# Performance work log

Measured on AMD Instinct MI355X. Metric: run time of the kernel, lower is better.

## Reference

```python
import jax, jax.numpy as jnp
import numpy as np

LAMBDA = 25.0
MU = 25.0
NU = 1.0
ALPHA = 0.25
EPS = 1e-4
NUM_MATCHES = (20, 4)


def _cdist(x, y):
    # x: (B, L1, C), y: (B, L2, C) -> (B, L1, L2) euclidean distances
    x2 = jnp.sum(x * x, axis=-1)[..., :, None]
    y2 = jnp.sum(y * y, axis=-1)[..., None, :]
    d2 = x2 + y2 - 2.0 * jnp.einsum('blc,bmc->blm', x, y)
    return jnp.sqrt(jnp.maximum(d2, 0.0))


def _nearest_neighbors(input_maps, candidate_maps, distances, num_matches):
    # For each input location, its nearest candidate; then keep the
    # num_matches input locations with smallest NN distance, in original order.
    nn_dist = jnp.min(distances, axis=-1)    # (B, L1)
    nn_idx = jnp.argmin(distances, axis=-1)  # (B, L1)
    _, sel = jax.lax.top_k(-nn_dist, num_matches)  # (B, M) smallest distances
    sel = jnp.sort(sel, axis=1)  # restore original ordering of positions
    filtered_input = jnp.take_along_axis(input_maps, sel[..., None], axis=1)
    nn_sel = jnp.take_along_axis(nn_idx, sel, axis=1)
    filtered_candidate = jnp.take_along_axis(candidate_maps, nn_sel[..., None], axis=1)
    return filtered_input, filtered_candidate


def _mse(a, b):
    return jnp.mean((a - b) ** 2)


def _vicreg_loss(z_a, z_b):
    inv_loss = _mse(z_a, z_b)

    def var_loss(z):
        std = jnp.sqrt(jnp.var(z, axis=0, ddof=1) + EPS)
        return jnp.mean(jax.nn.relu(1.0 - std))

    def cov_loss(z):
        n, d = z.shape
        zc = z - jnp.mean(z, axis=0)
        cov = (zc.T @ zc) / (n - 1)
        off = cov - jnp.diag(jnp.diag(cov))
        return jnp.sum(off ** 2) / d

    v = 0.5 * (var_loss(z_a) + var_loss(z_b))
    c = cov_loss(z_a) + cov_loss(z_b)
    return LAMBDA * inv_loss + MU * v + NU * c


def _local_loss(z_global, z_local, grid_global, grid_local):
    B = z_global.shape[0]
    zg = z_global.reshape(B, -1, z_global.shape[-1])   # (B, Lg, C)
    zl = z_local.reshape(B, -1, z_local.shape[-1])     # (B, Ll, C)

    inv_loss = 0.0
    # feature-space NN
    gf, gn = _nearest_neighbors(zg, zl, _cdist(zg, zl), NUM_MATCHES[0])
    lf, ln = _nearest_neighbors(zl, zg, _cdist(zl, zg), NUM_MATCHES[1])
    inv_loss = inv_loss + (_mse(gf, gn) / 2 + _mse(lf, ln) / 2)

    # grid-space NN (distances from grids, gather from feature maps)
    gg = grid_global.reshape(B, -1, 2)
    gl = grid_local.reshape(B, -1, 2)
    gf, gn = _nearest_neighbors(zg, zl, _cdist(gg, gl), NUM_MATCHES[0])
    lf, ln = _nearest_neighbors(zl, zg, _cdist(gl, gg), NUM_MATCHES[1])
    inv_loss = inv_loss + (_mse(gf, gn) / 2 + _mse(lf, ln) / 2)

    return LAMBDA * inv_loss


def setup_inputs() -> dict:
    key = jax.random.key(0)
    ks = jax.random.split(key, 6)
    B, D, C = 32, 8192, 512
    return {
        'z_global': jax.random.normal(ks[0], (B, D), jnp.float32),
        'z_local': jax.random.normal(ks[1], (B, D), jnp.float32),
        'z_global_local_features': jax.random.normal(ks[2], (B, 24, 24, C), jnp.float32),
        'z_local_local_features': jax.random.normal(ks[3], (B, 16, 16, C), jnp.float32),
        'grid_global': jax.random.uniform(ks[4], (B, 24, 24, 2), jnp.float32),
        'grid_local': jax.random.uniform(ks[5], (B, 16, 16, 2), jnp.float32),
    }


def reference(z_global, z_local, z_global_local_features, z_local_local_features, grid_global, grid_local):
    global_loss = _vicreg_loss(z_global, z_local)
    local_loss = _local_loss(z_global_local_features, z_local_local_features, grid_global, grid_local)
    return ALPHA * global_loss + (1.0 - ALPHA) * local_loss
```

## Files before the change

### kernel.cpp

```cpp
#include <hip/hip_runtime.h>
#include <hip/hip_bf16.h>

#define BATCH 32
#define DZ    8192
#define LG    576
#define LL    256
#define CH    512

#define OFF_S      0
#define OFF_BSUM   8192
#define OFF_SELSUM 9472
#define OFF_DONE   10496
#define OFF_NG     10560
#define OFF_NL     84288
#define OFF_ROWNN  117056
#define OFF_COLNN  264512
#define OFF_ABF    330048
#define OFF_BBF    19204416
#define WS_NEED    27593024

typedef __attribute__((ext_vector_type(8))) short bf16x8;
typedef __attribute__((ext_vector_type(4))) float f32x4;

__device__ __forceinline__ unsigned short f2bf(float x) {
  union { __hip_bfloat16 h; unsigned short u; } cv;
  cv.h = __float2bfloat16(x);
  return cv.u;
}

struct SelSmem {
  unsigned long long keys[LG];
  unsigned int nnm[LG];
  float cxy[2 * LG];
  unsigned int plist[40];
  unsigned int cnt;
  float fred[4];
};

template <int V>
__device__ __forceinline__ void sel_case(
    SelSmem& sm, int b,
    const float* __restrict__ zgf, const float* __restrict__ zlf,
    const float* __restrict__ gg, const float* __restrict__ gl,
    const unsigned long long* __restrict__ rowNN,
    const unsigned long long* __restrict__ colNN,
    double* __restrict__ selsum) {
  constexpr bool GDIR = (V == 0 || V == 2);
  constexpr int L1 = GDIR ? LG : LL;
  constexpr int L2 = GDIR ? LL : LG;
  constexpr int M  = GDIR ? 20 : 4;
  constexpr int NR = (L1 + 255) / 256;
  const float* fin  = GDIR ? zgf + (size_t)b * LG * CH : zlf + (size_t)b * LL * CH;
  const float* fcan = GDIR ? zlf + (size_t)b * LL * CH : zgf + (size_t)b * LG * CH;
  int tid = threadIdx.x, lane = tid & 63, wv = tid >> 6;
  if (tid == 0) sm.cnt = 0;

  if constexpr (V < 2) {
    const unsigned long long* src =
        (V == 0) ? rowNN + (size_t)b * LG : colNN + (size_t)b * LL;
    #pragma unroll
    for (int s = 0; s < NR; ++s) {
      int l = tid + s * 256;
      if (l < L1) {
        unsigned long long p = src[l];
        sm.keys[l] = (p & 0xFFFFFFFF00000000ull) | (unsigned)l;
        sm.nnm[l] = (unsigned)(p & 0xFFFFFFFFu);
      }
    }
  } else {
    const float* gin  = (V == 2) ? gg + (size_t)b * LG * 2 : gl + (size_t)b * LL * 2;
    const float* gcan = (V == 2) ? gl + (size_t)b * LL * 2 : gg + (size_t)b * LG * 2;
    #pragma unroll
    for (int s = 0; s < (2 * L2 + 255) / 256; ++s) {
      int i = tid + s * 256;
      if (i < 2 * L2) sm.cxy[i] = gcan[i];
    }
    __syncthreads();
    float x[NR], y[NR], bd[NR];
    unsigned bi[NR];
    #pragma unroll
    for (int s = 0; s < NR; ++s) {
      int l = tid + s * 256;
      x[s] = (l < L1) ? gin[2 * l] : 0.f;
      y[s] = (l < L1) ? gin[2 * l + 1] : 0.f;
      bd[s] = 3.4e38f; bi[s] = 0;
    }
    const float2* c2 = (const float2*)sm.cxy;
    for (int m2 = 0; m2 < L2; m2 += 8) {
      float2 cc[8];
      #pragma unroll
      for (int u = 0; u < 8; ++u) cc[u] = c2[m2 + u];
      #pragma unroll
      for (int u = 0; u < 8; ++u)
        #pragma unroll
        for (int s = 0; s < NR; ++s) {
          float dx = x[s] - cc[u].x, dy = y[s] - cc[u].y;
          float d2 = dx * dx + dy * dy;
          if (d2 < bd[s]) { bd[s] = d2; bi[s] = (unsigned)(m2 + u); }
        }
    }
    #pragma unroll
    for (int s = 0; s < NR; ++s) {
      int l = tid + s * 256;
      if (l < L1) {
        sm.keys[l] = ((unsigned long long)__float_as_uint(bd[s]) << 32) | (unsigned)l;
        sm.nnm[l] = bi[s];
      }
    }
  }
  __syncthreads();

  unsigned long long myk[NR];
  int rk[NR];
  #pragma unroll
  for (int s = 0; s < NR; ++s) {
    int l = tid + s * 256;
    myk[s] = (l < L1) ? sm.keys[l] : ~0ull;
    rk[s] = 0;
  }
  for (int j = 0; j < L1; j += 8) {
    unsigned long long kk[8];
    #pragma unroll
    for (int u = 0; u < 8; ++u) kk[u] = sm.keys[j + u];
    #pragma unroll
    for (int u = 0; u < 8; ++u)
      #pragma unroll
      for (int s = 0; s < NR; ++s) rk[s] += (kk[u] < myk[s]) ? 1 : 0;
  }
  #pragma unroll
  for (int s = 0; s < NR; ++s) {
    int l = tid + s * 256;
    if (l < L1 && rk[s] < M) {
      unsigned slot = atomicAdd(&sm.cnt, 1u);
      sm.plist[2 * slot] = (unsigned)l;
      sm.plist[2 * slot + 1] = sm.nnm[l];
    }
  }
  __syncthreads();

  float part = 0.f;
  #pragma unroll
  for (int rr = 0; rr < M / 4; ++rr) {
    int r = wv + rr * 4;
    const float4* a4 = (const float4*)(fin + (size_t)sm.plist[2 * r] * CH);
    const float4* c4 = (const float4*)(fcan + (size_t)sm.plist[2 * r + 1] * CH);
    float4 xa = a4[lane * 2], xb = a4[lane * 2 + 1];
    float4 ya = c4[lane * 2], yb = c4[lane * 2 + 1];
    float d0 = xa.x - ya.x, d1 = xa.y - ya.y, d2 = xa.z - ya.z, d3 = xa.w - ya.w;
    float d4 = xb.x - yb.x, d5 = xb.y - yb.y, d6 = xb.z - yb.z, d7 = xb.w - yb.w;
    part += d0 * d0 + d1 * d1 + d2 * d2 + d3 * d3 +
            d4 * d4 + d5 * d5 + d6 * d6 + d7 * d7;
  }
  for (int s = 32; s; s >>= 1) part += __shfl_down(part, s);
  if (lane == 0) sm.fred[wv] = part;
  __syncthreads();
  if (tid == 0)
    selsum[V * 32 + b] = (double)(sm.fred[0] + sm.fred[1] + sm.fred[2] + sm.fred[3]);
}

__global__ __launch_bounds__(256) void k_front(
    const float* __restrict__ za, const float* __restrict__ zb,
    const float* __restrict__ zgf, const float* __restrict__ zlf,
    const float* __restrict__ gg, const float* __restrict__ gl,
    double* __restrict__ bsum, float* __restrict__ S,
    unsigned short* __restrict__ Abf, unsigned short* __restrict__ Bbf,
    float* __restrict__ ng, float* __restrict__ nl,
    unsigned long long* __restrict__ nnInit,
    double* __restrict__ selsum, unsigned* __restrict__ done, int do_bf16) {
  __shared__ float sred[4][8];
  __shared__ SelSmem sm;
  int tid = threadIdx.x, lane = tid & 63, wv = tid >> 6;
  int blk = blockIdx.x;

  if (blk < 64) {
    if (blk == 0 && tid == 0) *done = 0u;
    int b = blk & 31;
    if (blk >> 5)
      sel_case<3>(sm, b, zgf, zlf, gg, gl, nnInit, nnInit, selsum);
    else
      sel_case<2>(sm, b, zgf, zlf, gg, gl, nnInit, nnInit, selsum);
  } else if (blk < 96) {
    int sblk = blk - 64;
    int i = sblk * 256 + tid;
    float sa = 0.f, qa = 0.f, sb = 0.f, qb = 0.f, si = 0.f;
    #pragma unroll 8
    for (int b = 0; b < BATCH; ++b) {
      float va = za[(size_t)b * DZ + i];
      float vb = zb[(size_t)b * DZ + i];
      sa += va; qa += va * va;
      sb += vb; qb += vb * vb;
      float d = va - vb; si += d * d;
    }
    float ssa = qa - sa * sa * (1.f / 32.f);
    float ssb = qb - sb * sb * (1.f / 32.f);
    float v0 = si;
    float v1 = fmaxf(0.f, 1.f - sqrtf(ssa * (1.f / 31.f) + 1e-4f));
    float v2 = fmaxf(0.f, 1.f - sqrtf(ssb * (1.f / 31.f) + 1e-4f));
    float v3 = ssa * ssa, v4 = ssb * ssb;
    for (int off = 32; off; off >>= 1) {
      v0 += __shfl_down(v0, off); v1 += __shfl_down(v1, off);
      v2 += __shfl_down(v2, off); v3 += __shfl_down(v3, off);
      v4 += __shfl_down(v4, off);
    }
    if (lane == 0) {
      sred[wv][0] = v0; sred[wv][1] = v1; sred[wv][2] = v2;
      sred[wv][3] = v3; sred[wv][4] = v4;
    }
    __syncthreads();
    if (tid < 5)
      bsum[sblk * 5 + tid] =
          (double)(sred[0][tid] + sred[1][tid] + sred[2][tid] + sred[3][tid]);
  } else if (blk < 1152) {
    int e = blk - 96;
    int zi = e >= 528; if (zi) e -= 528;
    const float* z = zi ? zb : za;
    float* Sz = S + zi * 1024;
    int p = 0, rem = e;
    while (rem >= 32 - p) { rem -= 32 - p; ++p; }
    int q = p + rem;
    const float4* zp = (const float4*)(z + (size_t)p * DZ);
    const float4* zq = (const float4*)(z + (size_t)q * DZ);
    float s = 0.f;
    #pragma unroll
    for (int ii = 0; ii < 8; ++ii) {
      int i = tid + ii * 256;
      float4 a = zp[i], b = zq[i];
      s += a.x * b.x + a.y * b.y + a.z * b.z + a.w * b.w;
    }
    for (int off = 32; off; off >>= 1) s += __shfl_down(s, off);
    if (lane == 0) sred[wv][0] = s;
    __syncthreads();
    if (tid == 0) {
      float r = sred[0][0] + sred[1][0] + sred[2][0] + sred[3][0];
      Sz[p * 32 + q] = r;
      if (p != q) Sz[q * 32 + p] = r;
    }
  } else {
    int rbase = (blk - 1152) * 16 + wv * 4;
    if (lane < 4) nnInit[rbase + lane] = ~0ull;
    const float* srcs[4]; unsigned short* dsts[4]; float* nrms[4];
    #pragma unroll
    for (int r = 0; r < 4; ++r) {
      int row = rbase + r;
      if (row < BATCH * LG) {
        srcs[r] = zgf + (size_t)row * CH; dsts[r] = Abf + (size_t)row * CH;
        nrms[r] = ng + row;
      } else {
        int rr = row - BATCH * LG;
        srcs[r] = zlf + (size_t)rr * CH; dsts[r] = Bbf + (size_t)rr * CH;
        nrms[r] = nl + rr;
      }
    }
    float4 v0[4], v1[4];
    #pragma unroll
    for (int r = 0; r < 4; ++r) {
      const float4* s4 = (const float4*)srcs[r];
      v0[r] = s4[lane * 2];
      v1[r] = s4[lane * 2 + 1];
    }
    #pragma unroll
    for (int r = 0; r < 4; ++r) {
      float ss = v0[r].x * v0[r].x + v0[r].y * v0[r].y + v0[r].z * v0[r].z +
                 v0[r].w * v0[r].w + v1[r].x * v1[r].x + v1[r].y * v1[r].y +
                 v1[r].z * v1[r].z + v1[r].w * v1[r].w;
      if (do_bf16) {
        union { unsigned short h[8]; uint4 u; } pk;
        pk.h[0] = f2bf(v0[r].x); pk.h[1] = f2bf(v0[r].y);
        pk.h[2] = f2bf(v0[r].z); pk.h[3] = f2bf(v0[r].w);
        pk.h[4] = f2bf(v1[r].x); pk.h[5] = f2bf(v1[r].y);
        pk.h[6] = f2bf(v1[r].z); pk.h[7] = f2bf(v1[r].w);
        *(uint4*)(dsts[r] + lane * 8) = pk.u;
      }
      for (int off = 32; off; off >>= 1) ss += __shfl_down(ss, off);
      if (lane == 0) *nrms[r] = ss;
    }
  }
}

__global__ __launch_bounds__(256) void k_feat_mfma(
    const unsigned short* __restrict__ Abf, const unsigned short* __restrict__ Bbf,
    const float* __restrict__ ng, const float* __restrict__ nl,
    unsigned long long* __restrict__ rowNN, unsigned long long* __restrict__ colNN) {
  const int b = blockIdx.z;
  const int row0 = blockIdx.x * 64;
  const int col0 = blockIdx.y * 64;
  const int tid = threadIdx.x;
  const int wave = tid >> 6, lane = tid & 63;
  const int m16 = lane & 15, quad = lane >> 4;
  const int wm = wave >> 1, wn = wave & 1;

  __shared__ unsigned short As[64][72];
  __shared__ unsigned short Bs[64][72];

  const unsigned short* Ag = Abf + ((size_t)(b * LG + row0)) * CH;
  const unsigned short* Bg = Bbf + ((size_t)(b * LL + col0)) * CH;

  const int sr = tid >> 2;
  const int sq = tid & 3;

  f32x4 acc[2][2] = {};

  for (int k0 = 0; k0 < CH; k0 += 64) {
    uint4 a0 = *(const uint4*)(Ag + (size_t)sr * CH + k0 + sq * 16);
    uint4 a1 = *(const uint4*)(Ag + (size_t)sr * CH + k0 + sq * 16 + 8);
    uint4 b0 = *(const uint4*)(Bg + (size_t)sr * CH + k0 + sq * 16);
    uint4 b1 = *(const uint4*)(Bg + (size_t)sr * CH + k0 + sq * 16 + 8);
    __syncthreads();
    *(uint4*)&As[sr][sq * 16] = a0; *(uint4*)&As[sr][sq * 16 + 8] = a1;
    *(uint4*)&Bs[sr][sq * 16] = b0; *(uint4*)&Bs[sr][sq * 16 + 8] = b1;
    __syncthreads();
    #pragma unroll
    for (int kk = 0; kk < 64; kk += 32) {
      bf16x8 af0 = *(const bf16x8*)&As[wm * 32 + m16][kk + quad * 8];
      bf16x8 af1 = *(const bf16x8*)&As[wm * 32 + 16 + m16][kk + quad * 8];
      bf16x8 bf0 = *(const bf16x8*)&Bs[wn * 32 + m16][kk + quad * 8];
      bf16x8 bf1 = *(const bf16x8*)&Bs[wn * 32 + 16 + m16][kk + quad * 8];
      acc[0][0] = __builtin_amdgcn_mfma_f32_16x16x32_bf16(af0, bf0, acc[0][0], 0, 0, 0);
      acc[0][1] = __builtin_amdgcn_mfma_f32_16x16x32_bf16(af0, bf1, acc[0][1], 0, 0, 0);
      acc[1][0] = __builtin_amdgcn_mfma_f32_16x16x32_bf16(af1, bf0, acc[1][0], 0, 0, 0);
      acc[1][1] = __builtin_amdgcn_mfma_f32_16x16x32_bf16(af1, bf1, acc[1][1], 0, 0, 0);
    }
  }

  float na[2][4], nb[2];
  #pragma unroll
  for (int i = 0; i < 2; ++i)
    #pragma unroll
    for (int r = 0; r < 4; ++r)
      na[i][r] = ng[b * LG + row0 + wm * 32 + i * 16 + quad * 4 + r];
  #pragma unroll
  for (int j = 0; j < 2; ++j)
    nb[j] = nl[b * LL + col0 + wn * 32 + j * 16 + m16];

  #pragma unroll
  for (int i = 0; i < 2; ++i) {
    #pragma unroll
    for (int r = 0; r < 4; ++r) {
      float d0 = fmaxf(na[i][r] + nb[0] - 2.f * acc[i][0][r], 0.f);
      float d1 = fmaxf(na[i][r] + nb[1] - 2.f * acc[i][1][r], 0.f);
      unsigned c0 = (unsigned)(col0 + wn * 32 + m16);
      unsigned long long p0 = (((unsigned long long)__float_as_uint(d0)) << 32) | c0;
      unsigned long long p1 = (((unsigned long long)__float_as_uint(d1)) << 32) | (c0 + 16);
      unsigned long long p = p0 < p1 ? p0 : p1;
      #pragma unroll
      for (int s = 1; s < 16; s <<= 1) {
        unsigned long long q = __shfl_xor(p, s);
        p = q < p ? q : p;
      }
      if (m16 == 0)
        atomicMin(&rowNN[(size_t)b * LG + row0 + wm * 32 + i * 16 + quad * 4 + r], p);
    }
  }
  #pragma unroll
  for (int j = 0; j < 2; ++j) {
    unsigned long long p = ~0ull;
    #pragma unroll
    for (int i = 0; i < 2; ++i) {
      #pragma unroll
      for (int r = 0; r < 4; ++r) {
        float d = fmaxf(na[i][r] + nb[j] - 2.f * acc[i][j][r], 0.f);
        unsigned rg = (unsigned)(row0 + wm * 32 + i * 16 + quad * 4 + r);
        unsigned long long pr = (((unsigned long long)__float_as_uint(d)) << 32) | rg;
        p = pr < p ? pr : p;
      }
    }
    unsigned long long q = __shfl_xor(p, 16); p = q < p ? q : p;
    q = __shfl_xor(p, 32); p = q < p ? q : p;
    if (quad == 0)
      atomicMin(&colNN[(size_t)b * LL + col0 + wn * 32 + j * 16 + m16], p);
  }
}

__global__ __launch_bounds__(256) void k_feat_nn(
    const float* __restrict__ zgf, const float* __restrict__ zlf,
    const float* __restrict__ ng, const float* __restrict__ nl,
    unsigned long long* __restrict__ rowNN, unsigned long long* __restrict__ colNN) {
  const int b = blockIdx.z;
  const int row0 = blockIdx.x * 64;
  const int col0 = blockIdx.y * 128;
  const int tid = threadIdx.x;
  const int tx = tid & 15, ty = tid >> 4;
  __shared__ float As[64][20];
  __shared__ float Bs[128][20];
  __shared__ float Ds[64][130];
  const float* Ag = zgf + ((size_t)b * LG + row0) * CH;
  const float* Bg = zlf + ((size_t)b * LL + col0) * CH;
  float acc[4][8];
  #pragma unroll
  for (int i = 0; i < 4; ++i)
    #pragma unroll
    for (int j = 0; j < 8; ++j) acc[i][j] = 0.f;
  const int ar = tid >> 2;
  const int ak = (tid & 3) * 4;
  for (int k0 = 0; k0 < CH; k0 += 16) {
    float4 av  = *(const float4*)(Ag + (size_t)ar * CH + k0 + ak);
    float4 bv0 = *(const float4*)(Bg + (size_t)ar * CH + k0 + ak);
    float4 bv1 = *(const float4*)(Bg + (size_t)(ar + 64) * CH + k0 + ak);
    __syncthreads();
    *(float4*)&As[ar][ak] = av;
    *(float4*)&Bs[ar][ak] = bv0;
    *(float4*)&Bs[ar + 64][ak] = bv1;
    __syncthreads();
    #pragma unroll
    for (int k = 0; k < 16; ++k) {
      float a0 = As[ty][k], a1 = As[ty + 16][k], a2 = As[ty + 32][k], a3 = As[ty + 48][k];
      float bv[8];
      #pragma unroll
      for (int j = 0; j < 8; ++j) bv[j] = Bs[tx + 16 * j][k];
      #pragma unroll
      for (int j = 0; j < 8; ++j) {
        acc[0][j] += a0 * bv[j]; acc[1][j] += a1 * bv[j];
        acc[2][j] += a2 * bv[j]; acc[3][j] += a3 * bv[j];
      }
    }
  }
  float ngr[4], nlc[8];
  #pragma unroll
  for (int i = 0; i < 4; ++i) ngr[i] = ng[b * LG + row0 + ty + 16 * i];
  #pragma unroll
  for (int j = 0; j < 8; ++j) nlc[j] = nl[b * LL + col0 + tx + 16 * j];
  #pragma unroll
  for (int i = 0; i < 4; ++i)
    #pragma unroll
    for (int j = 0; j < 8; ++j)
      Ds[ty + 16 * i][tx + 16 * j] = fmaxf(ngr[i] + nlc[j] - 2.f * acc[i][j], 0.f);
  __syncthreads();
  if (tid < 64) {
    unsigned long long best = ~0ull;
    for (int c = 0; c < 128; ++c) {
      unsigned long long p =
          ((unsigned long long)__float_as_uint(Ds[tid][c]) << 32) | (unsigned)(col0 + c);
      best = p < best ? p : best;
    }
    atomicMin(&rowNN[(size_t)b * LG + row0 + tid], best);
  } else if (tid < 192) {
    int c = tid - 64;
    unsigned long long best = ~0ull;
    for (int r = 0; r < 64; ++r) {
      unsigned long long p =
          ((unsigned long long)__float_as_uint(Ds[r][c]) << 32) | (unsigned)(row0 + r);
      best = p < best ? p : best;
    }
    atomicMin(&colNN[(size_t)b * LL + col0 + c], best);
  }
}

__global__ __launch_bounds__(256) void k_sel(
    const float* __restrict__ zgf, const float* __restrict__ zlf,
    const float* __restrict__ gg, const float* __restrict__ gl,
    const unsigned long long* __restrict__ rowNN,
    const unsigned long long* __restrict__ colNN,
    double* __restrict__ selsum, const double* __restrict__ bsum,
    const float* __restrict__ S, unsigned* __restrict__ done,
    float* __restrict__ out) {
  __shared__ SelSmem sm;
  int b = blockIdx.x;
  if (blockIdx.y == 0)
    sel_case<0>(sm, b, zgf, zlf, gg, gl, rowNN, colNN, selsum);
  else
    sel_case<1>(sm, b, zgf, zlf, gg, gl, rowNN, colNN, selsum);

  __shared__ unsigned isLast;
  __shared__ float t[2][32];
  __shared__ double sacc[5];
  __shared__ double smf[4];
  __shared__ double totred[2];
  int tid = threadIdx.x, lane = tid & 63, wv = tid >> 6;
  if (tid == 0) {
    __threadfence();
    unsigned old = __hip_atomic_fetch_add(done, 1u, __ATOMIC_ACQ_REL,
                                          __HIP_MEMORY_SCOPE_AGENT);
    isLast = (old == 63u) ? 1u : 0u;
  }
  __syncthreads();
  if (isLast) {
    __threadfence();
    if (tid < 64) {
      int zi = tid >> 5, p = tid & 31;
      float tp = 0.f;
      for (int bb = 0; bb < 32; ++bb) tp += S[zi * 1024 + p * 32 + bb];
      t[zi][p] = tp * (1.f / 32.f);
    } else if (tid < 69) {
      int k = tid - 64;
      double s = 0.0;
      for (int blk = 0; blk < 32; ++blk) s += bsum[blk * 5 + k];
      sacc[k] = s;
    } else if (tid >= 72 && tid < 76) {
      int v = tid - 72;
      double s = 0.0;
      for (int bb = 0; bb < 32; ++bb) s += selsum[v * 32 + bb];
      smf[v] = s;
    }
    __syncthreads();
    if (wv < 2) {
      int zi = wv;
      float u = 0.f;
      for (int bb = 0; bb < 32; ++bb) u += t[zi][bb];
      u *= (1.f / 32.f);
      double s = 0.0;
      for (int e = lane; e < 1024; e += 64) {
        int p = e >> 5, q = e & 31;
        float G = S[zi * 1024 + e] - t[zi][p] - t[zi][q] + u;
        s += (double)G * (double)G;
      }
      for (int off = 32; off; off >>= 1) s += __shfl_down(s, off);
      if (lane == 0) totred[zi] = s;
    }
    __syncthreads();
    if (tid == 0) {
      double inv_g = sacc[0] / (32.0 * 8192.0);
      double v = 0.5 * (sacc[1] + sacc[2]) / 8192.0;
      double c = (totred[0] - sacc[3] + totred[1] - sacc[4]) / (961.0 * 8192.0);
      double gloss = 25.0 * inv_g + 25.0 * v + c;
      double mfg = smf[0] / (32.0 * 20.0 * 512.0);
      double mfl = smf[1] / (32.0 * 4.0 * 512.0);
      double mgg = smf[2] / (32.0 * 20.0 * 512.0);
      double mgl = smf[3] / (32.0 * 4.0 * 512.0);
      double lloss = 25.0 * (0.5 * (mfg + mfl) + 0.5 * (mgg + mgl));
      out[0] = (float)(0.25 * gloss + 0.75 * lloss);
    }
  }
}

extern "C" void kernel_launch(void* const* d_in, const int* in_sizes, int n_in,
                              void* d_out, int out_size, void* d_ws, size_t ws_size,
                              hipStream_t stream) {
  const float* zg  = (const float*)d_in[0];
  const float* zl  = (const float*)d_in[1];
  const float* zgf = (const float*)d_in[2];
  const float* zlf = (const float*)d_in[3];
  const float* gg  = (const float*)d_in[4];
  const float* glo = (const float*)d_in[5];

  char* ws = (char*)d_ws;
  float* S       = (float*)(ws + OFF_S);
  double* bsum   = (double*)(ws + OFF_BSUM);
  double* selsum = (double*)(ws + OFF_SELSUM);
  unsigned* done = (unsigned*)(ws + OFF_DONE);
  float* ng = (float*)(ws + OFF_NG);
  float* nl = (float*)(ws + OFF_NL);
  unsigned long long* rowNN = (unsigned long long*)(ws + OFF_ROWNN);
  unsigned long long* colNN = (unsigned long long*)(ws + OFF_COLNN);
  unsigned short* Abf = (unsigned short*)(ws + OFF_ABF);
  unsigned short* Bbf = (unsigned short*)(ws + OFF_BBF);

  int do_bf16 = (ws_size >= WS_NEED) ? 1 : 0;

  k_front<<<2816, 256, 0, stream>>>(zg, zl, zgf, zlf, gg, glo, bsum, S,
                                    Abf, Bbf, ng, nl, rowNN, selsum, done, do_bf16);
  if (do_bf16) {
    k_feat_mfma<<<dim3(LG / 64, LL / 64, BATCH), 256, 0, stream>>>(
        Abf, Bbf, ng, nl, rowNN, colNN);
  } else {
    k_feat_nn<<<dim3(LG / 64, LL / 128, BATCH), 256, 0, stream>>>(
        zgf, zlf, ng, nl, rowNN, colNN);
  }
  k_sel<<<dim3(BATCH, 2), 256, 0, stream>>>(zgf, zlf, gg, glo, rowNN, colNN,
                                            selsum, bsum, S, done, (float*)d_out);
}
```

Before: 171.8 us.

## Fuse NN selection and final reduction into MFMA kernel via per-batch tail counters

The separate selection and finalize kernel is folded into the MFMA distance kernel. Each batch's last-finishing tile block (detected by an atomic counter per batch) runs the feature-space top-k selection and MSE for that batch, and a second counter picks the last batch to compute the final loss. This removes one kernel launch and lets selection for finished batches overlap with MFMA tiles of other batches. In exchange it adds atomics, fences and relaxed atomic loads, serializes both selection cases inside one block, and shares LDS through a union.

```diff
diff --git a/kernel.cpp b/kernel.cpp
--- a/kernel.cpp
+++ b/kernel.cpp
@@ -10,14 +10,14 @@
 #define OFF_S      0
 #define OFF_BSUM   8192
 #define OFF_SELSUM 9472
-#define OFF_DONE   10496
-#define OFF_NG     10560
-#define OFF_NL     84288
-#define OFF_ROWNN  117056
-#define OFF_COLNN  264512
-#define OFF_ABF    330048
-#define OFF_BBF    19204416
-#define WS_NEED    27593024
+#define OFF_CNT    10496
+#define OFF_NG     10752
+#define OFF_NL     84480
+#define OFF_ROWNN  117248
+#define OFF_COLNN  264704
+#define OFF_ABF    330240
+#define OFF_BBF    19204608
+#define WS_NEED    27593216
 
 typedef __attribute__((ext_vector_type(8))) short bf16x8;
 typedef __attribute__((ext_vector_type(4))) float f32x4;
@@ -26,6 +26,19 @@
   union { __hip_bfloat16 h; unsigned short u; } cv;
   cv.h = __float2bfloat16(x);
   return cv.u;
+}
+
+__device__ __forceinline__ unsigned long long ld_nn(const unsigned long long* p) {
+  return __hip_atomic_load(p, __ATOMIC_RELAXED, __HIP_MEMORY_SCOPE_AGENT);
+}
+__device__ __forceinline__ void st_sum(double* p, double v) {
+  __hip_atomic_store((unsigned long long*)p,
+                     (unsigned long long)__double_as_longlong(v),
+                     __ATOMIC_RELAXED, __HIP_MEMORY_SCOPE_AGENT);
+}
+__device__ __forceinline__ double ld_sum(const double* p) {
+  return __longlong_as_double((long long)__hip_atomic_load(
+      (const unsigned long long*)p, __ATOMIC_RELAXED, __HIP_MEMORY_SCOPE_AGENT));
 }
 
 struct SelSmem {
@@ -62,7 +75,7 @@
     for (int s = 0; s < NR; ++s) {
       int l = tid + s * 256;
       if (l < L1) {
-        unsigned long long p = src[l];
+        unsigned long long p = ld_nn(&src[l]);
         sm.keys[l] = (p & 0xFFFFFFFF00000000ull) | (unsigned)l;
         sm.nnm[l] = (unsigned)(p & 0xFFFFFFFFu);
       }
@@ -155,7 +168,9 @@
   if (lane == 0) sm.fred[wv] = part;
   __syncthreads();
   if (tid == 0)
-    selsum[V * 32 + b] = (double)(sm.fred[0] + sm.fred[1] + sm.fred[2] + sm.fred[3]);
+    st_sum(&selsum[V * 32 + b],
+           (double)(sm.fred[0] + sm.fred[1] + sm.fred[2] + sm.fred[3]));
+  __syncthreads();
 }
 
 __global__ __launch_bounds__(256) void k_front(
@@ -166,14 +181,14 @@
     unsigned short* __restrict__ Abf, unsigned short* __restrict__ Bbf,
     float* __restrict__ ng, float* __restrict__ nl,
     unsigned long long* __restrict__ nnInit,
-    double* __restrict__ selsum, unsigned* __restrict__ done, int do_bf16) {
+    double* __restrict__ selsum, unsigned* __restrict__ cnt, int do_bf16) {
   __shared__ float sred[4][8];
   __shared__ SelSmem sm;
   int tid = threadIdx.x, lane = tid & 63, wv = tid >> 6;
   int blk = blockIdx.x;
 
   if (blk < 64) {
-    if (blk == 0 && tid == 0) *done = 0u;
+    if (blk == 0 && tid < 34) cnt[tid] = 0u;
     int b = blk & 31;
     if (blk >> 5)
       sel_case<3>(sm, b, zgf, zlf, gg, gl, nnInit, nnInit, selsum);
@@ -277,10 +292,15 @@
   }
 }
 
-__global__ __launch_bounds__(256) void k_feat_mfma(
+__global__ __launch_bounds__(256) void k_mfma_sel(
     const unsigned short* __restrict__ Abf, const unsigned short* __restrict__ Bbf,
     const float* __restrict__ ng, const float* __restrict__ nl,
-    unsigned long long* __restrict__ rowNN, unsigned long long* __restrict__ colNN) {
+    const float* __restrict__ zgf, const float* __restrict__ zlf,
+    const float* __restrict__ gg, const float* __restrict__ gl,
+    unsigned long long* __restrict__ rowNN, unsigned long long* __restrict__ colNN,
+    double* __restrict__ selsum, const double* __restrict__ bsum,
+    const float* __restrict__ S, unsigned* __restrict__ cnt,
+    float* __restrict__ out) {
   const int b = blockIdx.z;
   const int row0 = blockIdx.x * 64;
   const int col0 = blockIdx.y * 64;
@@ -289,8 +309,13 @@
   const int m16 = lane & 15, quad = lane >> 4;
   const int wm = wave >> 1, wn = wave & 1;
 
-  __shared__ unsigned short As[64][72];
-  __shared__ unsigned short Bs[64][72];
+  __shared__ union {
+    struct { unsigned short As[64][72]; unsigned short Bs[64][72]; } m;
+    SelSmem s;
+  } u;
+  __shared__ unsigned tflag, fflag;
+  __shared__ float t[2][32];
+  __shared__ double sacc[5], smf[4], totred[2];
 
   const unsigned short* Ag = Abf + ((size_t)(b * LG + row0)) * CH;
   const unsigned short* Bg = Bbf + ((size_t)(b * LL + col0)) * CH;
@@ -306,15 +331,15 @@
     uint4 b0 = *(const uint4*)(Bg + (size_t)sr * CH + k0 + sq * 16);
     uint4 b1 = *(const uint4*)(Bg + (size_t)sr * CH + k0 + sq * 16 + 8);
     __syncthreads();
-    *(uint4*)&As[sr][sq * 16] = a0; *(uint4*)&As[sr][sq * 16 + 8] = a1;
-    *(uint4*)&Bs[sr][sq * 16] = b0; *(uint4*)&Bs[sr][sq * 16 + 8] = b1;
+    *(uint4*)&u.m.As[sr][sq * 16] = a0; *(uint4*)&u.m.As[sr][sq * 16 + 8] = a1;
+    *(uint4*)&u.m.Bs[sr][sq * 16] = b0; *(uint4*)&u.m.Bs[sr][sq * 16 + 8] = b1;
     __syncthreads();
     #pragma unroll
     for (int kk = 0; kk < 64; kk += 32) {
-      bf16x8 af0 = *(const bf16x8*)&As[wm * 32 + m16][kk + quad * 8];
-      bf16x8 af1 = *(const bf16x8*)&As[wm * 32 + 16 + m16][kk + quad * 8];
-      bf16x8 bf0 = *(const bf16x8*)&Bs[wn * 32 + m16][kk + quad * 8];
-      bf16x8 bf1 = *(const bf16x8*)&Bs[wn * 32 + 16 + m16][kk + quad * 8];
+      bf16x8 af0 = *(const bf16x8*)&u.m.As[wm * 32 + m16][kk + quad * 8];
+      bf16x8 af1 = *(const bf16x8*)&u.m.As[wm * 32 + 16 + m16][kk + quad * 8];
+      bf16x8 bf0 = *(const bf16x8*)&u.m.Bs[wn * 32 + m16][kk + quad * 8];
+      bf16x8 bf1 = *(const bf16x8*)&u.m.Bs[wn * 32 + 16 + m16][kk + quad * 8];
       acc[0][0] = __builtin_amdgcn_mfma_f32_16x16x32_bf16(af0, bf0, acc[0][0], 0, 0, 0);
       acc[0][1] = __builtin_amdgcn_mfma_f32_16x16x32_bf16(af0, bf1, acc[0][1], 0, 0, 0);
       acc[1][0] = __builtin_amdgcn_mfma_f32_16x16x32_bf16(af1, bf0, acc[1][0], 0, 0, 0);
@@ -368,6 +393,74 @@
     q = __shfl_xor(p, 32); p = q < p ? q : p;
     if (quad == 0)
       atomicMin(&colNN[(size_t)b * LL + col0 + wn * 32 + j * 16 + m16], p);
+  }
+
+  __threadfence();
+  __syncthreads();
+  if (tid == 0) {
+    unsigned old = __hip_atomic_fetch_add(&cnt[b], 1u, __ATOMIC_ACQ_REL,
+                                          __HIP_MEMORY_SCOPE_AGENT);
+    tflag = (old == 35u) ? 1u : 0u;
+  }
+  __syncthreads();
+  if (tflag) {
+    __threadfence();
+    sel_case<0>(u.s, b, zgf, zlf, gg, gl, rowNN, colNN, selsum);
+    sel_case<1>(u.s, b, zgf, zlf, gg, gl, rowNN, colNN, selsum);
+    __threadfence();
+    if (tid == 0) {
+      unsigned old2 = __hip_atomic_fetch_add(&cnt[32], 1u, __ATOMIC_ACQ_REL,
+                                             __HIP_MEMORY_SCOPE_AGENT);
+      fflag = (old2 == 31u) ? 1u : 0u;
+    }
+    __syncthreads();
+    if (fflag) {
+      __threadfence();
+      if (tid < 64) {
+        int zi = tid >> 5, p = tid & 31;
+        float tp = 0.f;
+        for (int bb = 0; bb < 32; ++bb) tp += S[zi * 1024 + p * 32 + bb];
+        t[zi][p] = tp * (1.f / 32.f);
+      } else if (tid < 69) {
+        int k = tid - 64;
+        double s = 0.0;
+        for (int blk = 0; blk < 32; ++blk) s += bsum[blk * 5 + k];
+        sacc[k] = s;
+      } else if (tid >= 72 && tid < 76) {
+        int v = tid - 72;
+        double s = 0.0;
+        for (int bb = 0; bb < 32; ++bb) s += ld_sum(&selsum[v * 32 + bb]);
+        smf[v] = s;
+      }
+      __syncthreads();
+      if (wave < 2) {
+        int zi = wave;
+        float uu = 0.f;
+        for (int bb = 0; bb < 32; ++bb) uu += t[zi][bb];
+        uu *= (1.f / 32.f);
+        double s = 0.0;
+        for (int e = lane; e < 1024; e += 64) {
+          int p = e >> 5, q = e & 31;
+          float G = S[zi * 1024 + e] - t[zi][p] - t[zi][q] + uu;
+          s += (double)G * (double)G;
+        }
+        for (int off = 32; off; off >>= 1) s += __shfl_down(s, off);
+        if (lane == 0) totred[zi] = s;
+      }
+      __syncthreads();
+      if (tid == 0) {
+        double inv_g = sacc[0] / (32.0 * 8192.0);
+        double v = 0.5 * (sacc[1] + sacc[2]) / 8192.0;
+        double c = (totred[0] - sacc[3] + totred[1] - sacc[4]) / (961.0 * 8192.0);
+        double gloss = 25.0 * inv_g + 25.0 * v + c;
+        double mfg = smf[0] / (32.0 * 20.0 * 512.0);
+        double mfl = smf[1] / (32.0 * 4.0 * 512.0);
+        double mgg = smf[2] / (32.0 * 20.0 * 512.0);
+        double mgl = smf[3] / (32.0 * 4.0 * 512.0);
+        double lloss = 25.0 * (0.5 * (mfg + mfl) + 0.5 * (mgg + mgl));
+        out[0] = (float)(0.25 * gloss + 0.75 * lloss);
+      }
+    }
   }
 }
 
@@ -445,7 +538,7 @@
   }
 }
 
-__global__ __launch_bounds__(256) void k_sel(
+__global__ __launch_bounds__(256) void k_sel_fb(
     const float* __restrict__ zgf, const float* __restrict__ zlf,
     const float* __restrict__ gg, const float* __restrict__ gl,
     const unsigned long long* __restrict__ rowNN,
@@ -462,9 +555,7 @@
 
   __shared__ unsigned isLast;
   __shared__ float t[2][32];
-  __shared__ double sacc[5];
-  __shared__ double smf[4];
-  __shared__ double totred[2];
+  __shared__ double sacc[5], smf[4], totred[2];
   int tid = threadIdx.x, lane = tid & 63, wv = tid >> 6;
   if (tid == 0) {
     __threadfence();
@@ -488,7 +579,7 @@
     } else if (tid >= 72 && tid < 76) {
       int v = tid - 72;
       double s = 0.0;
-      for (int bb = 0; bb < 32; ++bb) s += selsum[v * 32 + bb];
+      for (int bb = 0; bb < 32; ++bb) s += ld_sum(&selsum[v * 32 + bb]);
       smf[v] = s;
     }
     __syncthreads();
@@ -536,7 +627,7 @@
   float* S       = (float*)(ws + OFF_S);
   double* bsum   = (double*)(ws + OFF_BSUM);
   double* selsum = (double*)(ws + OFF_SELSUM);
-  unsigned* done = (unsigned*)(ws + OFF_DONE);
+  unsigned* cnt  = (unsigned*)(ws + OFF_CNT);
   float* ng = (float*)(ws + OFF_NG);
   float* nl = (float*)(ws + OFF_NL);
   unsigned long long* rowNN = (unsigned long long*)(ws + OFF_ROWNN);
@@ -547,14 +638,16 @@
   int do_bf16 = (ws_size >= WS_NEED) ? 1 : 0;
 
   k_front<<<2816, 256, 0, stream>>>(zg, zl, zgf, zlf, gg, glo, bsum, S,
-                                    Abf, Bbf, ng, nl, rowNN, selsum, done, do_bf16);
+                                    Abf, Bbf, ng, nl, rowNN, selsum, cnt, do_bf16);
   if (do_bf16) {
-    k_feat_mfma<<<dim3(LG / 64, LL / 64, BATCH), 256, 0, stream>>>(
-        Abf, Bbf, ng, nl, rowNN, colNN);
+    k_mfma_sel<<<dim3(LG / 64, LL / 64, BATCH), 256, 0, stream>>>(
+        Abf, Bbf, ng, nl, zgf, zlf, gg, glo, rowNN, colNN,
+        selsum, bsum, S, cnt, (float*)d_out);
   } else {
     k_feat_nn<<<dim3(LG / 64, LL / 128, BATCH), 256, 0, stream>>>(
         zgf, zlf, ng, nl, rowNN, colNN);
-  }
-  k_sel<<<dim3(BATCH, 2), 256, 0, stream>>>(zgf, zlf, gg, glo, rowNN, colNN,
-                                            selsum, bsum, S, done, (float*)d_out);
-}
+    k_sel_fb<<<dim3(BATCH, 2), 256, 0, stream>>>(zgf, zlf, gg, glo, rowNN, colNN,
+                                                 selsum, bsum, S, cnt + 33,
+                                                 (float*)d_out);
+  }
+}
```

Measured after the change: 269.5 us. +56.8%, slower.
